# Optimization experiments

Measured on AMD Instinct MI355X. Metric: run time of the kernel, lower is better.

## Reference

```python
import jax, jax.numpy as jnp
import numpy as np

# Dims (match init_kwargs / input_specs)
N, N_REP, K, D = 8, 2048, 16, 3
C_IN, C_LIFT = 64, 64
C_MID = C_IN + C_LIFT   # 128
C_OUT = 128             # groups=C_OUT -> depthwise since C_MID == C_OUT
EPS = 1e-5


def setup_inputs() -> dict:
    key = jax.random.key(0)
    ks = jax.random.split(key, 10)
    w = lambda i, shape, fan_in: (jax.random.uniform(ks[i], shape, dtype=jnp.float32) * 2.0 - 1.0) / np.float32(np.sqrt(fan_in))
    return dict(
        p=jax.random.normal(ks[0], (N, N_REP, D), dtype=jnp.float32),
        P=jax.random.normal(ks[1], (N, N_REP, K, D), dtype=jnp.float32),
        F=jax.random.normal(ks[2], (N, N_REP, K, C_IN), dtype=jnp.float32),
        # BatchNorm over the D spatial channels (training-mode stats)
        bn_gamma=jnp.ones((D,), dtype=jnp.float32),
        bn_beta=jnp.zeros((D,), dtype=jnp.float32),
        # mlp_lift: Dense(D->C_LIFT) + Dense(C_LIFT->C_LIFT), ELU each
        lift_w1=w(3, (D, C_LIFT), D), lift_b1=jnp.zeros((C_LIFT,), dtype=jnp.float32),
        lift_w2=w(4, (C_LIFT, C_LIFT), C_LIFT), lift_b2=jnp.zeros((C_LIFT,), dtype=jnp.float32),
        # mid_conv: 1x1 Conv2d(D -> K) channels-last == Linear on last dim
        mid_w=w(5, (D, K), D), mid_b=jnp.zeros((K,), dtype=jnp.float32),
        # mlp: Dense(K->K) with ELU
        mlp_w=w(6, (K, K), K), mlp_b=jnp.zeros((K,), dtype=jnp.float32),
        # end_conv: Conv2d(C_MID -> C_OUT, kernel (K,1), groups=C_OUT) == depthwise
        # reduction over the neighbor dim; weight per (out_channel, neighbor)
        end_w=w(7, (C_OUT, K), K), end_b=jnp.zeros((C_OUT,), dtype=jnp.float32),
    )


def reference(p, P, F, bn_gamma, bn_beta, lift_w1, lift_b1, lift_w2, lift_b2,
              mid_w, mid_b, mlp_w, mlp_b, end_w, end_b):
    # Center neighborhoods on the representative point
    P_local = P - p[:, :, None, :]                              # (N,R,K,D)
    # Channels-last BatchNorm over D, batch stats over (N,R,K)
    mean = jnp.mean(P_local, axis=(0, 1, 2), keepdims=True)
    var = jnp.var(P_local, axis=(0, 1, 2), keepdims=True)
    P_norm = (P_local - mean) * jax.lax.rsqrt(var + EPS) * bn_gamma + bn_beta
    # Lift spatial coords to C_LIFT features (MLP of Dense+ELU layers)
    F_lift = jax.nn.elu(P_norm @ lift_w1 + lift_b1)
    F_lift = jax.nn.elu(F_lift @ lift_w2 + lift_b2)             # (N,R,K,C_LIFT)
    F_cat = jnp.concatenate([F_lift, F], axis=-1)               # (N,R,K,C_MID)
    # X-transform: 1x1 conv D->K then Dense(K->K)+ELU -> (N,R,K,K)
    X = P_norm @ mid_w + mid_b
    X = jax.nn.elu(X @ mlp_w + mlp_b)
    # Weighted aggregation: small batched matmul over the neighbor dim
    F_X = jnp.einsum('nrkj,nrjc->nrkc', X, F_cat)               # (N,R,K,C_MID)
    # Depthwise end conv: per-channel weighted sum over neighbors
    F_p = jnp.einsum('nrkc,ck->nrc', F_X, end_w) + end_b        # (N,R,C_OUT)
    return F_p
```

## Files before the change

kernel.cpp:

```cpp
#include <hip/hip_runtime.h>
#include <cstddef>

#define N_TOT   8
#define R_TOT   2048
#define KK      16
#define CL      64
#define CM      128
#define EPSV    1e-5f
#define CNTF    262144.0f

typedef float    f32x4  __attribute__((ext_vector_type(4)));
typedef short    bf16x8 __attribute__((ext_vector_type(8)));
typedef unsigned u32x4  __attribute__((ext_vector_type(4)));

union FragU { bf16x8 f; unsigned u[4]; };

__device__ float    g_w1f[72*4];
__device__ unsigned g_w2p[8*64*4];
__device__ float    g_bn[8];
__device__ unsigned g_cnt = 0;

__device__ __forceinline__ float elu_f(float x){
    return x > 0.f ? x : (__expf(x) - 1.f);
}

#if defined(__has_builtin) && __has_builtin(__builtin_amdgcn_cvt_pk_bf16_f32)
__device__ __forceinline__ unsigned pk_bf16(float a, float b){
    auto v = __builtin_amdgcn_cvt_pk_bf16_f32(a, b);
    unsigned u; __builtin_memcpy(&u, &v, 4);
    return u;
}
#else
__device__ __forceinline__ unsigned pk_bf16(float a, float b){
    unsigned ua = __float_as_uint(a), ub = __float_as_uint(b);
    ua += 0x7fff + ((ua >> 16) & 1);
    ub += 0x7fff + ((ub >> 16) & 1);
    return (ua >> 16) | (ub & 0xffff0000u);
}
#endif
__device__ __forceinline__ float bf_lo(unsigned u){ return __uint_as_float(u << 16); }
__device__ __forceinline__ float bf_hi(unsigned u){ return __uint_as_float(u & 0xffff0000u); }

__device__ __forceinline__ void split4(const float* x, unsigned* o){
    unsigned h01 = pk_bf16(x[0], x[1]);
    unsigned h23 = pk_bf16(x[2], x[3]);
    float l0 = x[0] - bf_lo(h01), l1 = x[1] - bf_hi(h01);
    float l2 = x[2] - bf_lo(h23), l3 = x[3] - bf_hi(h23);
    o[0] = h01; o[1] = h23; o[2] = pk_bf16(l0, l1); o[3] = pk_bf16(l2, l3);
}

__global__ __launch_bounds__(256) void xconv_stats(
    const float* __restrict__ p, const float* __restrict__ P,
    const float* __restrict__ w1, const float* __restrict__ b1,
    const float* __restrict__ w2,
    const float* __restrict__ gamma, const float* __restrict__ beta,
    float* __restrict__ ws)
{
    const int tid = threadIdx.x;
    const int g = blockIdx.x*256 + tid;
    const float4* P4 = (const float4*)(P + (size_t)g*12);
    float4 a = P4[0], b = P4[1], c = P4[2];
    const int nr = g >> 2;
    float pp0 = p[nr*3], pp1 = p[nr*3+1], pp2 = p[nr*3+2];
    float vx0=a.x-pp0, vx1=a.w-pp0, vx2=b.z-pp0, vx3=c.y-pp0;
    float vy0=a.y-pp1, vy1=b.x-pp1, vy2=b.w-pp1, vy3=c.z-pp1;
    float vz0=a.z-pp2, vz1=b.y-pp2, vz2=c.x-pp2, vz3=c.w-pp2;
    float s1[3], s2[3];
    s1[0]=vx0+vx1+vx2+vx3; s2[0]=vx0*vx0+vx1*vx1+vx2*vx2+vx3*vx3;
    s1[1]=vy0+vy1+vy2+vy3; s2[1]=vy0*vy0+vy1*vy1+vy2*vy2+vy3*vy3;
    s1[2]=vz0+vz1+vz2+vz3; s2[2]=vz0*vz0+vz1*vz1+vz2*vz2+vz3*vz3;

    #pragma unroll
    for (int off = 32; off > 0; off >>= 1){
        #pragma unroll
        for (int d = 0; d < 3; d++){
            s1[d] += __shfl_down(s1[d], off, 64);
            s2[d] += __shfl_down(s2[d], off, 64);
        }
    }
    __shared__ float red[4][6];
    __shared__ int   sLast;
    int wave = tid >> 6, lane = tid & 63;
    if (lane == 0){
        #pragma unroll
        for (int d = 0; d < 3; d++){ red[wave][d] = s1[d]; red[wave][3+d] = s2[d]; }
    }
    __syncthreads();
    if (tid < 8){
        float v = 0.f;
        if (tid < 6) v = red[0][tid] + red[1][tid] + red[2][tid] + red[3][tid];
        ws[blockIdx.x*8 + tid] = v;
        __threadfence();
    }

    if (blockIdx.x == 0){
        if (wave == 0){
            f32x4 w4 = { w1[lane], w1[64+lane], w1[128+lane], b1[lane] };
            *(f32x4*)&g_w1f[((lane>>3)*9 + (lane&7))*4] = w4;
        } else if (wave == 1){
            const int lo16 = lane & 15, quad = lane >> 4;
            #pragma unroll
            for (int bb = 0; bb < 4; bb++)
                #pragma unroll
                for (int s = 0; s < 2; s++){
                    u32x4 f;
                    #pragma unroll
                    for (int d = 0; d < 4; d++){
                        int q0 = s*32 + quad*8 + d*2;
                        int idx = q0*64 + bb*16 + lo16;
                        f[d] = pk_bf16(w2[idx], w2[idx + 64]);
                    }
                    *(u32x4*)&g_w2p[((bb*2 + s)*64 + lane)*4] = f;
                }
        }
    }

    __syncthreads();
    if (tid == 0){
        unsigned old = atomicAdd(&g_cnt, 1u);
        sLast = (old == 255u);
        if (sLast) atomicExch(&g_cnt, 0u);
    }
    __syncthreads();
    if (sLast && tid < 64){
        __threadfence();
        float t1[3] = {0.f,0.f,0.f}, t2[3] = {0.f,0.f,0.f};
        const f32x4* wp = (const f32x4*)ws;
        #pragma unroll
        for (int i = 0; i < 4; i++){
            int row = tid + i*64;
            f32x4 pa = wp[row*2], pb = wp[row*2 + 1];
            t1[0] += pa.x; t1[1] += pa.y; t1[2] += pa.z;
            t2[0] += pa.w; t2[1] += pb.x; t2[2] += pb.y;
        }
        #pragma unroll
        for (int off = 32; off > 0; off >>= 1){
            #pragma unroll
            for (int d = 0; d < 3; d++){
                t1[d] += __shfl_xor(t1[d], off, 64);
                t2[d] += __shfl_xor(t2[d], off, 64);
            }
        }
        if (tid == 0){
            #pragma unroll
            for (int d = 0; d < 3; d++){
                float mean = t1[d] * (1.0f/CNTF);
                float var  = t2[d] * (1.0f/CNTF) - mean*mean;
                float s    = gamma[d] * rsqrtf(var + EPSV);
                g_bn[d] = s; g_bn[3+d] = beta[d] - mean*s;
            }
            g_bn[6] = 0.f; g_bn[7] = 0.f;
        }
    }
}

__global__ __launch_bounds__(256, 5) void xconv_main(
    const float* __restrict__ p,   const float* __restrict__ P,
    const float* __restrict__ F,
    const float* __restrict__ mlpw,const float* __restrict__ mlpb,
    const float* __restrict__ midw,const float* __restrict__ midb,
    const float* __restrict__ b2,
    const float* __restrict__ endw,const float* __restrict__ endb,
    float* __restrict__ out)
{
    __shared__ float    sEndw[128*20];
    __shared__ float    sW1f[72*4];
    __shared__ unsigned sW2[8*64*4];
    __shared__ float    sMid[16*4];

    const int tid  = threadIdx.x;
    const int lane = tid & 63;
    const int lo16 = lane & 15;
    const int quad = lane >> 4;
    const int wave = tid >> 6;

    if (wave == 0){
        *(f32x4*)&sW1f[lane*4] = *(const f32x4*)&g_w1f[lane*4];
        if (lane < 8)
            *(f32x4*)&sW1f[(64+lane)*4] = *(const f32x4*)&g_w1f[(64+lane)*4];
    } else if (wave == 1){
        #pragma unroll
        for (int i = 0; i < 8; i++)
            *(u32x4*)&sW2[(i*64+lane)*4] = *(const u32x4*)&g_w2p[(i*64+lane)*4];
    } else {
        int c = tid - 128;
        int row = (c < 64) ? c : 64 + ((c-64)&3)*16 + ((c-64)>>2);
        const f32x4* ep = (const f32x4*)endw;
        #pragma unroll
        for (int i = 0; i < 4; i++)
            *(f32x4*)&sEndw[row*20 + i*4] = ep[c*4 + i];
        if (c >= 112){
            int m2 = c - 112;
            f32x4 mv = { midw[m2], midw[16+m2], midw[32+m2], midb[m2] };
            *(f32x4*)&sMid[m2*4] = mv;
        }
    }

    f32x4 bn0 = *(const f32x4*)&g_bn[0];
    float sc0 = bn0.x, sc1 = bn0.y, sc2 = bn0.z, sh0 = bn0.w;
    float sh1 = g_bn[4], sh2 = g_bn[5];

    FragU mlpA[2];
    {
        float mw[4];
        #pragma unroll
        for (int r = 0; r < 4; r++) mw[r] = mlpw[(quad*4 + r)*16 + lo16];
        unsigned o[4]; split4(mw, o);
        mlpA[0].u[0]=o[0]; mlpA[0].u[1]=o[1]; mlpA[0].u[2]=o[0]; mlpA[0].u[3]=o[1];
        mlpA[1].u[0]=o[2]; mlpA[1].u[1]=o[3]; mlpA[1].u[2]=o[2]; mlpA[1].u[3]=o[3];
    }
    float mlpbr[4];
    #pragma unroll
    for (int r = 0; r < 4; r++) mlpbr[r] = mlpb[quad*4 + r];
    float b2r[4];
    #pragma unroll
    for (int b = 0; b < 4; b++) b2r[b] = b2[b*16 + lo16];
    const float endb0 = endb[lane], endb1 = endb[64 + lane];

    __syncthreads();

    const int nr = blockIdx.x*4 + wave;

    const int pb = nr*48 + lo16*3;
    float P0 = P[pb], P1 = P[pb+1], P2 = P[pb+2];
    float pp0 = p[nr*3], pp1 = p[nr*3+1], pp2 = p[nr*3+2];

    const float4* fp = (const float4*)(F + (size_t)nr*1024 + (size_t)(quad*4)*64);
    float4 q0 = fp[lo16], q1 = fp[16+lo16], q2 = fp[32+lo16], q3 = fp[48+lo16];
    unsigned fh01[4] = { pk_bf16(q0.x,q1.x), pk_bf16(q0.y,q1.y),
                         pk_bf16(q0.z,q1.z), pk_bf16(q0.w,q1.w) };
    unsigned fh23[4] = { pk_bf16(q2.x,q3.x), pk_bf16(q2.y,q3.y),
                         pk_bf16(q2.z,q3.z), pk_bf16(q2.w,q3.w) };

    const float pn0 = (P0 - pp0)*sc0 + sh0;
    const float pn1 = (P1 - pp1)*sc1 + sh1;
    const float pn2 = (P2 - pp2)*sc2 + sh2;

    FragU hf[2];
    #pragma unroll
    for (int s = 0; s < 2; s++){
        const f32x4* wp = (const f32x4*)&sW1f[((s*4 + quad)*9)*4];
        #pragma unroll
        for (int d = 0; d < 4; d++){
            f32x4 wa = wp[2*d], wb = wp[2*d+1];
            float h0  = fmaf(pn2, wa.z, fmaf(pn1, wa.y, fmaf(pn0, wa.x, wa.w)));
            float h1v = fmaf(pn2, wb.z, fmaf(pn1, wb.y, fmaf(pn0, wb.x, wb.w)));
            hf[s].u[d] = pk_bf16(elu_f(h0), elu_f(h1v));
        }
    }

    float x0[4];
    #pragma unroll
    for (int j = 0; j < 4; j++){
        f32x4 mw = *(const f32x4*)&sMid[(quad*4 + j)*4];
        x0[j] = fmaf(pn2, mw.z, fmaf(pn1, mw.y, fmaf(pn0, mw.x, mw.w)));
    }
    FragU x0f; split4(x0, x0f.u);

    f32x4 dx = {0.f,0.f,0.f,0.f};
    dx = __builtin_amdgcn_mfma_f32_16x16x32_bf16(mlpA[0].f, x0f.f, dx, 0,0,0);
    dx = __builtin_amdgcn_mfma_f32_16x16x32_bf16(mlpA[1].f, x0f.f, dx, 0,0,0);
    float xv[4];
    #pragma unroll
    for (int r = 0; r < 4; r++) xv[r] = elu_f(dx[r] + mlpbr[r]);
    FragU xA; split4(xv, xA.u);

    float o0 = 0.f;

    #pragma unroll
    for (int b = 0; b < 4; b++){
        FragU wf0, wf1;
        *(u32x4*)wf0.u = *(const u32x4*)&sW2[((b*2 + 0)*64 + lane)*4];
        *(u32x4*)wf1.u = *(const u32x4*)&sW2[((b*2 + 1)*64 + lane)*4];
        f32x4 dl = {0.f,0.f,0.f,0.f};
        dl = __builtin_amdgcn_mfma_f32_16x16x32_bf16(hf[0].f, wf0.f, dl, 0,0,0);
        dl = __builtin_amdgcn_mfma_f32_16x16x32_bf16(hf[1].f, wf1.f, dl, 0,0,0);
        float fl[4];
        #pragma unroll
        for (int r = 0; r < 4; r++) fl[r] = elu_f(dl[r] + b2r[b]);
        FragU bfg;
        unsigned h01 = pk_bf16(fl[0], fl[1]), h23 = pk_bf16(fl[2], fl[3]);
        bfg.u[0] = h01; bfg.u[1] = h23; bfg.u[2] = h01; bfg.u[3] = h23;
        f32x4 da = {0.f,0.f,0.f,0.f};
        da = __builtin_amdgcn_mfma_f32_16x16x32_bf16(xA.f, bfg.f, da, 0,0,0);
        const float4 ew = *(const float4*)&sEndw[(b*16 + lo16)*20 + quad*4];
        float pt = da[0]*ew.x + da[1]*ew.y + da[2]*ew.z + da[3]*ew.w;
        pt += __shfl_xor(pt, 16, 64);
        pt += __shfl_xor(pt, 32, 64);
        if (b == quad) o0 = pt;
    }
    float pt4[4];
    #pragma unroll
    for (int g = 0; g < 4; g++){
        FragU bfg;
        bfg.u[0] = fh01[g]; bfg.u[1] = fh23[g];
        bfg.u[2] = fh01[g]; bfg.u[3] = fh23[g];
        f32x4 da = {0.f,0.f,0.f,0.f};
        da = __builtin_amdgcn_mfma_f32_16x16x32_bf16(xA.f, bfg.f, da, 0,0,0);
        const float4 ew = *(const float4*)&sEndw[(64 + g*16 + lo16)*20 + quad*4];
        float pt = da[0]*ew.x + da[1]*ew.y + da[2]*ew.z + da[3]*ew.w;
        pt += __shfl_xor(pt, 16, 64);
        pt += __shfl_xor(pt, 32, 64);
        pt4[g] = pt;
    }
    const int src = quad*20 + (lo16 >> 2);
    float t0 = __shfl(pt4[0], src, 64), t1 = __shfl(pt4[1], src, 64);
    float t2 = __shfl(pt4[2], src, 64), t3 = __shfl(pt4[3], src, 64);
    float ta = (lo16 & 1) ? t1 : t0;
    float tb = (lo16 & 1) ? t3 : t2;
    float o1 = (lo16 & 2) ? tb : ta;

    out[(size_t)nr*CM + lane]      = o0 + endb0;
    out[(size_t)nr*CM + 64 + lane] = o1 + endb1;
}

extern "C" void kernel_launch(void* const* d_in, const int* in_sizes, int n_in,
                              void* d_out, int out_size, void* d_ws, size_t ws_size,
                              hipStream_t stream)
{
    const float* p     = (const float*)d_in[0];
    const float* P     = (const float*)d_in[1];
    const float* F     = (const float*)d_in[2];
    const float* gamma = (const float*)d_in[3];
    const float* beta  = (const float*)d_in[4];
    const float* w1    = (const float*)d_in[5];
    const float* b1    = (const float*)d_in[6];
    const float* w2    = (const float*)d_in[7];
    const float* b2    = (const float*)d_in[8];
    const float* midw  = (const float*)d_in[9];
    const float* midb  = (const float*)d_in[10];
    const float* mlpw  = (const float*)d_in[11];
    const float* mlpb  = (const float*)d_in[12];
    const float* endw  = (const float*)d_in[13];
    const float* endb  = (const float*)d_in[14];
    float* ws  = (float*)d_ws;
    float* out = (float*)d_out;

    xconv_stats<<<256, 256, 0, stream>>>(p, P, w1, b1, w2, gamma, beta, ws);
    xconv_main <<<4096, 256, 0, stream>>>(p, P, F, mlpw, mlpb, midw, midb,
                                          b2, endw, endb, out);
}
```

Measured before the change: 142.6 us.

## Load F channels contiguously per lane and drop end-weight row permutation and shuffles

F is now read so that each lane takes the contiguous channel bt*16+lo16 for four neighbors, instead of float4 vectors that interleaved channels. This makes the MFMA output channel order natural, so the permuted end-weight layout in shared memory and the four __shfl gathers with select logic are removed. The launch bound rises from 5 to 6 blocks per SIMD, which caps register use. The trade-off is scalar 4-byte global loads in place of 16-byte vector loads, and possible register pressure or spills under the tighter bound.

```diff
diff --git a/kernel.cpp b/kernel.cpp
--- a/kernel.cpp
+++ b/kernel.cpp
@@ -154,7 +154,7 @@
     }
 }
 
-__global__ __launch_bounds__(256, 5) void xconv_main(
+__global__ __launch_bounds__(256, 6) void xconv_main(
     const float* __restrict__ p,   const float* __restrict__ P,
     const float* __restrict__ F,
     const float* __restrict__ mlpw,const float* __restrict__ mlpb,
@@ -184,11 +184,10 @@
             *(u32x4*)&sW2[(i*64+lane)*4] = *(const u32x4*)&g_w2p[(i*64+lane)*4];
     } else {
         int c = tid - 128;
-        int row = (c < 64) ? c : 64 + ((c-64)&3)*16 + ((c-64)>>2);
         const f32x4* ep = (const f32x4*)endw;
         #pragma unroll
         for (int i = 0; i < 4; i++)
-            *(f32x4*)&sEndw[row*20 + i*4] = ep[c*4 + i];
+            *(f32x4*)&sEndw[c*20 + i*4] = ep[c*4 + i];
         if (c >= 112){
             int m2 = c - 112;
             f32x4 mv = { midw[m2], midw[16+m2], midw[32+m2], midb[m2] };
@@ -225,12 +224,14 @@
     float P0 = P[pb], P1 = P[pb+1], P2 = P[pb+2];
     float pp0 = p[nr*3], pp1 = p[nr*3+1], pp2 = p[nr*3+2];
 
-    const float4* fp = (const float4*)(F + (size_t)nr*1024 + (size_t)(quad*4)*64);
-    float4 q0 = fp[lo16], q1 = fp[16+lo16], q2 = fp[32+lo16], q3 = fp[48+lo16];
-    unsigned fh01[4] = { pk_bf16(q0.x,q1.x), pk_bf16(q0.y,q1.y),
-                         pk_bf16(q0.z,q1.z), pk_bf16(q0.w,q1.w) };
-    unsigned fh23[4] = { pk_bf16(q2.x,q3.x), pk_bf16(q2.y,q3.y),
-                         pk_bf16(q2.z,q3.z), pk_bf16(q2.w,q3.w) };
+    unsigned fh01[4], fh23[4];
+    #pragma unroll
+    for (int bt = 0; bt < 4; bt++){
+        const size_t fb = (size_t)nr*1024 + (size_t)(quad*4)*64 + bt*16 + lo16;
+        float f0 = F[fb], f1 = F[fb + 64], f2 = F[fb + 128], f3 = F[fb + 192];
+        fh01[bt] = pk_bf16(f0, f1);
+        fh23[bt] = pk_bf16(f2, f3);
+    }
 
     const float pn0 = (P0 - pp0)*sc0 + sh0;
     const float pn1 = (P1 - pp1)*sc1 + sh1;
@@ -265,7 +266,7 @@
     for (int r = 0; r < 4; r++) xv[r] = elu_f(dx[r] + mlpbr[r]);
     FragU xA; split4(xv, xA.u);
 
-    float o0 = 0.f;
+    float o0 = 0.f, o1 = 0.f;
 
     #pragma unroll
     for (int b = 0; b < 4; b++){
@@ -289,26 +290,19 @@
         pt += __shfl_xor(pt, 32, 64);
         if (b == quad) o0 = pt;
     }
-    float pt4[4];
-    #pragma unroll
-    for (int g = 0; g < 4; g++){
+    #pragma unroll
+    for (int bt = 0; bt < 4; bt++){
         FragU bfg;
-        bfg.u[0] = fh01[g]; bfg.u[1] = fh23[g];
-        bfg.u[2] = fh01[g]; bfg.u[3] = fh23[g];
+        bfg.u[0] = fh01[bt]; bfg.u[1] = fh23[bt];
+        bfg.u[2] = fh01[bt]; bfg.u[3] = fh23[bt];
         f32x4 da = {0.f,0.f,0.f,0.f};
         da = __builtin_amdgcn_mfma_f32_16x16x32_bf16(xA.f, bfg.f, da, 0,0,0);
-        const float4 ew = *(const float4*)&sEndw[(64 + g*16 + lo16)*20 + quad*4];
+        const float4 ew = *(const float4*)&sEndw[(64 + bt*16 + lo16)*20 + quad*4];
         float pt = da[0]*ew.x + da[1]*ew.y + da[2]*ew.z + da[3]*ew.w;
         pt += __shfl_xor(pt, 16, 64);
         pt += __shfl_xor(pt, 32, 64);
-        pt4[g] = pt;
-    }
-    const int src = quad*20 + (lo16 >> 2);
-    float t0 = __shfl(pt4[0], src, 64), t1 = __shfl(pt4[1], src, 64);
-    float t2 = __shfl(pt4[2], src, 64), t3 = __shfl(pt4[3], src, 64);
-    float ta = (lo16 & 1) ? t1 : t0;
-    float tb = (lo16 & 1) ? t3 : t2;
-    float o1 = (lo16 & 2) ? tb : ta;
+        if (bt == quad) o1 = pt;
+    }
 
     out[(size_t)nr*CM + lane]      = o0 + endb0;
     out[(size_t)nr*CM + 64 + lane] = o1 + endb1;
```

New measurement: 140.1 us. Within noise of the previous version (-1.8%).
